# Optimization experiments

Measured on AMD Instinct MI355X. Metric: run time of the kernel, lower is better.

Reference implementation:

```python
import jax, jax.numpy as jnp
import numpy as np

B, C, H, W = 4, 64, 64, 64


def setup_inputs() -> dict:
    key = jax.random.key(0)
    ks = jax.random.split(key, 9)
    s = 1.0 / np.sqrt(C)
    return {
        "x1": jax.random.normal(ks[0], (B, C, H, W), dtype=jnp.float32),
        "x2": jax.random.normal(ks[1], (B, C, H, W), dtype=jnp.float32),
        "wq": jax.random.normal(ks[2], (C, C), dtype=jnp.float32) * s,
        "bq": jax.random.normal(ks[3], (C,), dtype=jnp.float32) * 0.01,
        "wk": jax.random.normal(ks[4], (C, C), dtype=jnp.float32) * s,
        "bk": jax.random.normal(ks[5], (C,), dtype=jnp.float32) * 0.01,
        "wv": jax.random.normal(ks[6], (C, C), dtype=jnp.float32) * s,
        "bv": jax.random.normal(ks[7], (C,), dtype=jnp.float32) * 0.01,
        "gamma": jax.random.normal(ks[8], (1,), dtype=jnp.float32) * 0.1,
    }


def _conv1x1(x, w, b):
    # 1x1 conv == per-pixel GEMM: [B,C,H,W] x [Cout,Cin] -> [B,Cout,H,W]
    return jnp.einsum('bchw,oc->bohw', x, w) + b[None, :, None, None]


def reference(x1, x2, wq, bq, wk, bk, wv, bv, gamma):
    b, c, h, w = x1.shape
    n = h * w
    q = _conv1x1(x1, wq, bq).reshape(b, c, n)   # [B,C,N]
    k = _conv1x1(x2, wk, bk).reshape(b, c, n)   # [B,C,N]
    v = _conv1x1(x2, wv, bv).reshape(b, c, n)   # [B,C,N]
    # attention[b,i,j] = sum_c q[b,c,i] * k[b,c,j]  -> [B,N,N]
    attn = jnp.einsum('bci,bcj->bij', q, k)
    attn = jax.nn.softmax(attn, axis=-1)
    # out[b,c,i] = sum_j v[b,c,j] * attn[b,i,j]
    out = jnp.einsum('bcj,bij->bci', v, attn).reshape(b, c, h, w)
    return gamma[0] * out + x1
```

## Files before the change

### kernel.cpp

```cpp
#include <hip/hip_runtime.h>
#include <cstdint>
#include <cstddef>


typedef __bf16 bf16x4 __attribute__((ext_vector_type(4)));
typedef __bf16 bf16x8 __attribute__((ext_vector_type(8)));
typedef float  f32x4  __attribute__((ext_vector_type(4)));
typedef float  f32x16 __attribute__((ext_vector_type(16)));
typedef short  s16x4  __attribute__((ext_vector_type(4)));

constexpr int C = 64;
constexpr int N = 4096;
constexpr float LOG2E = 1.44269504088896340736f;
constexpr float EXPSHIFT = 48.0f * 1.44269504088896340736f;

static __device__ __forceinline__ f32x4 mfma16(bf16x8 a, bf16x8 b, f32x4 c) {
    return __builtin_amdgcn_mfma_f32_16x16x32_bf16(a, b, c, 0, 0, 0);
}
static __device__ __forceinline__ f32x16 mfma32(bf16x8 a, bf16x8 b, f32x16 c) {
    return __builtin_amdgcn_mfma_f32_32x32x16_bf16(a, b, c, 0, 0, 0);
}
static __device__ __forceinline__ f32x16 pv_mfma(bf16x4 a, bf16x4 b, f32x16 c) {
#if __has_builtin(__builtin_amdgcn_mfma_f32_32x32x8bf16_1k)
    union U { bf16x4 h; s16x4 s; };
    U ua; ua.h = a;
    U ub; ub.h = b;
    return __builtin_amdgcn_mfma_f32_32x32x8bf16_1k(ua.s, ub.s, c, 0, 0, 0);
#else
    const __bf16 z = (__bf16)0.0f;
    bf16x8 a8 = {a[0], a[1], a[2], a[3], z, z, z, z};
    bf16x8 b8 = {b[0], b[1], b[2], b[3], z, z, z, z};
    return __builtin_amdgcn_mfma_f32_32x32x16_bf16(a8, b8, c, 0, 0, 0);
#endif
}
static __device__ __forceinline__ float fast_exp2(float x) {
#if __has_builtin(__builtin_amdgcn_exp2f)
    return __builtin_amdgcn_exp2f(x);
#else
    return exp2f(x);
#endif
}

__global__ __launch_bounds__(256) void qkv_kernel(
    const float* __restrict__ x1, const float* __restrict__ x2,
    const float* __restrict__ wq, const float* __restrict__ bq,
    const float* __restrict__ wk, const float* __restrict__ bk,
    const float* __restrict__ wv, const float* __restrict__ bv,
    __bf16* __restrict__ qo, __bf16* __restrict__ ko, __bf16* __restrict__ vo)
{
    __shared__ __bf16 wl[3][64][72];

    const int tid   = threadIdx.x;
    const int b     = blockIdx.x >> 6;
    const int nbase = (blockIdx.x & 63) * 64;

    {
        const float* wp[3] = {wq, wk, wv};
#pragma unroll
        for (int m = 0; m < 3; ++m)
#pragma unroll
            for (int i = 0; i < 4; ++i) {
                int idx = i * 256 + tid;
                int row = idx >> 4, c4 = (idx & 15) * 4;
                float4 a = *(const float4*)(wp[m] + row * 64 + c4);
                bf16x4 h = {(__bf16)a.x, (__bf16)a.y, (__bf16)a.z, (__bf16)a.w};
                *(bf16x4*)&wl[m][row][c4] = h;
            }
    }
    __syncthreads();

    const int wave = tid >> 6, lane = tid & 63;
    const int l = lane & 15, qd = lane >> 4;
    const int p = nbase + wave * 16 + l;

    const float* x1b = x1 + (size_t)b * C * N + p;
    const float* x2b = x2 + (size_t)b * C * N + p;
    bf16x8 ax1[2], ax2[2];
#pragma unroll
    for (int ks = 0; ks < 2; ++ks)
#pragma unroll
        for (int j = 0; j < 8; ++j) {
            int c = ks * 32 + qd * 8 + j;
            ax1[ks][j] = (__bf16)x1b[(size_t)c * N];
            ax2[ks][j] = (__bf16)x2b[(size_t)c * N];
        }

    const size_t tb = ((size_t)b * 128 + (nbase >> 5) + (wave >> 1)) * 2048;

#pragma unroll
    for (int ot = 0; ot < 4; ++ot) {
        const float bqv = bq[ot * 16 + l];
        const float bkv = bk[ot * 16 + l];
        f32x4 aq = {bqv, bqv, bqv, bqv};
        f32x4 ak = {bkv, bkv, bkv, bkv};
#pragma unroll
        for (int ks = 0; ks < 2; ++ks) {
            bf16x8 bwq = *(const bf16x8*)&wl[0][ot * 16 + l][ks * 32 + qd * 8];
            bf16x8 bwk = *(const bf16x8*)&wl[1][ot * 16 + l][ks * 32 + qd * 8];
            aq = mfma16(ax1[ks], bwq, aq);
            ak = mfma16(ax2[ks], bwk, ak);
        }
#pragma unroll
        for (int r = 0; r < 4; ++r) {
            int p32 = (wave & 1) * 16 + qd * 4 + r;
            size_t idx = tb + ot * 512 + (l >> 3) * 256 + p32 * 8 + (l & 7);
            qo[idx] = (__bf16)(aq[r] * LOG2E);
            ko[idx] = (__bf16)ak[r];
        }
    }

    const int kcs = ((wave & 1) * 16 + l) >> 3;
    const int vhi = (l >> 2) & 1;
#pragma unroll
    for (int ct = 0; ct < 4; ++ct) {
        f32x4 av;
#pragma unroll
        for (int r = 0; r < 4; ++r) av[r] = bv[ct * 16 + qd * 4 + r];
#pragma unroll
        for (int ks = 0; ks < 2; ++ks) {
            bf16x8 awv = *(const bf16x8*)&wl[2][ct * 16 + l][ks * 32 + qd * 8];
            av = mfma16(awv, ax2[ks], av);
        }
#pragma unroll
        for (int r = 0; r < 4; ++r) {
            int o = ct * 16 + qd * 4 + r;
            vo[tb + kcs * 512 + vhi * 256 + o * 4 + (l & 3)] = (__bf16)av[r];
        }
    }
}

__global__ __launch_bounds__(512, 2) void attn_kernel(
    const __bf16* __restrict__ qg, const __bf16* __restrict__ kg,
    const __bf16* __restrict__ vg, const float* __restrict__ x1,
    const float* __restrict__ gamma, float* __restrict__ out)
{
    __shared__ float lds_acc[3][64][64];
    __shared__ float lds_l[8][64];

    const int bid = blockIdx.x;
    const int xcd = bid & 7;
    const int b   = xcd >> 1;
    const int rt  = ((bid >> 3) << 1) | (xcd & 1);
    const int ibase = rt * 64;

    const int tid  = threadIdx.x;
    const int wave = tid >> 6, lane = tid & 63;
    const int il = lane & 31, hi = lane >> 5;

    const __bf16* qt = qg + ((size_t)b * 128 + rt * 2) * 2048;
    const __bf16* kt = kg + (size_t)b * 128 * 2048 + (size_t)(wave * 16) * 2048;
    const __bf16* vt = vg + (size_t)b * 128 * 2048 + (size_t)(wave * 16) * 2048;

    bf16x8 bqf[2][4];
#pragma unroll
    for (int qs = 0; qs < 2; ++qs)
#pragma unroll
        for (int kc = 0; kc < 4; ++kc)
            bqf[qs][kc] = *(const bf16x8*)(qt + qs * 2048 + kc * 512 + lane * 8);

    f32x16 accO[4];
#pragma unroll
    for (int a = 0; a < 4; ++a)
#pragma unroll
        for (int r = 0; r < 16; ++r) accO[a][r] = 0.f;
    float lsum[2] = {0.f, 0.f};

    bf16x8 akf[2][4];
    bf16x4 avf[2][4];

#pragma unroll
    for (int kc = 0; kc < 4; ++kc)
        akf[0][kc] = *(const bf16x8*)(kt + kc * 512 + lane * 8);

#pragma unroll 4
    for (int t = 0; t < 16; ++t) {
        const int cur = t & 1;
        if (t < 15) {
#pragma unroll
            for (int kc = 0; kc < 4; ++kc)
                akf[cur ^ 1][kc] = *(const bf16x8*)(kt + (size_t)(t + 1) * 2048 + kc * 512 + lane * 8);
        }
#pragma unroll
        for (int ct = 0; ct < 2; ++ct)
#pragma unroll
            for (int kcs = 0; kcs < 4; ++kcs)
                avf[ct][kcs] = *(const bf16x4*)(vt + (size_t)t * 2048 + kcs * 512 + hi * 256 + ct * 128 + il * 4);

#pragma unroll
        for (int qs = 0; qs < 2; ++qs) {
            f32x16 st;
#pragma unroll
            for (int r = 0; r < 16; ++r) st[r] = 0.f;
#pragma unroll
            for (int kc = 0; kc < 4; ++kc) st = mfma32(akf[cur][kc], bqf[qs][kc], st);

            bf16x4 bp[4];
            float ls = 0.f;
#pragma unroll
            for (int r = 0; r < 16; ++r) {
                float pv = fast_exp2(st[r] - EXPSHIFT);
                ls += pv;
                bp[r >> 2][r & 3] = (__bf16)pv;
            }
            lsum[qs] += ls;

#pragma unroll
            for (int ct = 0; ct < 2; ++ct)
#pragma unroll
                for (int kcs = 0; kcs < 4; ++kcs)
                    accO[qs * 2 + ct] = pv_mfma(avf[ct][kcs], bp[kcs], accO[qs * 2 + ct]);
        }
    }

#pragma unroll
    for (int qs = 0; qs < 2; ++qs) lsum[qs] += __shfl_xor(lsum[qs], 32);
    if (hi == 0) {
        lds_l[wave][il]      = lsum[0];
        lds_l[wave][32 + il] = lsum[1];
    }

#define ACC_STORE(SLOT)                                                        \
    do {                                                                       \
        _Pragma("unroll")                                                      \
        for (int qs = 0; qs < 2; ++qs)                                         \
            _Pragma("unroll")                                                  \
            for (int ct = 0; ct < 2; ++ct)                                     \
                _Pragma("unroll")                                              \
                for (int r = 0; r < 16; ++r)                                   \
                    lds_acc[SLOT][ct * 32 + (r & 3) + 8 * (r >> 2) + 4 * hi][qs * 32 + il] = accO[qs * 2 + ct][r]; \
    } while (0)
#define ACC_LOAD(SLOT)                                                         \
    do {                                                                       \
        _Pragma("unroll")                                                      \
        for (int qs = 0; qs < 2; ++qs)                                         \
            _Pragma("unroll")                                                  \
            for (int ct = 0; ct < 2; ++ct)                                     \
                _Pragma("unroll")                                              \
                for (int r = 0; r < 16; ++r)                                   \
                    accO[qs * 2 + ct][r] += lds_acc[SLOT][ct * 32 + (r & 3) + 8 * (r >> 2) + 4 * hi][qs * 32 + il]; \
    } while (0)

    if (wave >= 5) ACC_STORE(wave - 5);
    __syncthreads();
    if (wave >= 1 && wave <= 3) ACC_LOAD(wave - 1);
    __syncthreads();
    if (wave >= 2 && wave <= 4) ACC_STORE(wave - 2);
    __syncthreads();
    if (wave <= 1) ACC_LOAD(wave);
    if (wave == 0) ACC_LOAD(2);
    __syncthreads();
    if (wave == 1) ACC_STORE(0);
    __syncthreads();
    if (wave == 0) { ACC_LOAD(0); ACC_STORE(0); }
    __syncthreads();
#undef ACC_STORE
#undef ACC_LOAD

    const float g = gamma[0];
    {
        const int c  = tid >> 3;
        const int i8 = (tid & 7) * 8;
        float lv[8];
#pragma unroll
        for (int e = 0; e < 8; ++e) {
            float s = 0.f;
#pragma unroll
            for (int w = 0; w < 8; ++w) s += lds_l[w][i8 + e];
            lv[e] = s;
        }
        const size_t idx = ((size_t)b * C + c) * N + ibase + i8;
        f32x4 o0 = *(const f32x4*)&lds_acc[0][c][i8];
        f32x4 o1 = *(const f32x4*)&lds_acc[0][c][i8 + 4];
        f32x4 x0 = *(const f32x4*)(x1 + idx);
        f32x4 x4 = *(const f32x4*)(x1 + idx + 4);
        f32x4 r0, r1;
#pragma unroll
        for (int e = 0; e < 4; ++e) {
            r0[e] = g * o0[e] / lv[e] + x0[e];
            r1[e] = g * o1[e] / lv[4 + e] + x4[e];
        }
        *(f32x4*)(out + idx) = r0;
        *(f32x4*)(out + idx + 4) = r1;
    }
}

extern "C" void kernel_launch(void* const* d_in, const int* in_sizes, int n_in,
                              void* d_out, int out_size, void* d_ws, size_t ws_size,
                              hipStream_t stream) {
    const float* x1    = (const float*)d_in[0];
    const float* x2    = (const float*)d_in[1];
    const float* wq    = (const float*)d_in[2];
    const float* bqv   = (const float*)d_in[3];
    const float* wk    = (const float*)d_in[4];
    const float* bkv   = (const float*)d_in[5];
    const float* wv    = (const float*)d_in[6];
    const float* bvv   = (const float*)d_in[7];
    const float* gamma = (const float*)d_in[8];
    float* out = (float*)d_out;

    __bf16* qws = (__bf16*)d_ws;
    __bf16* kws = qws + (size_t)4 * 128 * 2048;
    __bf16* vws = kws + (size_t)4 * 128 * 2048;

    qkv_kernel<<<256, 256, 0, stream>>>(x1, x2, wq, bqv, wk, bkv, wv, bvv, qws, kws, vws);
    attn_kernel<<<256, 512, 0, stream>>>(qws, kws, vws, x1, gamma, out);
}
```

Measured before the change: 104.6 us.

## Split attention KV range across blocks and reduce partials in an epilogue kernel

The attention kernel moves from 256 blocks of 8 waves, each covering all keys for one 64-query tile, to 1024 blocks of 4 waves, each covering a quarter of the keys. Each block writes unnormalized partial outputs and row sums to workspace, and a new epilogue kernel sums the four splits, normalizes, and applies the gamma residual. Q fragments are now staged through LDS rather than held in registers, which lowers register pressure so three blocks can fit per CU. The goal is more parallelism and occupancy. The cost is an extra kernel launch, about 16MB of partial-output traffic through global memory, and extra LDS reads for Q.

```diff
diff --git a/kernel.cpp b/kernel.cpp
--- a/kernel.cpp
+++ b/kernel.cpp
@@ -129,34 +129,36 @@
     }
 }
 
-__global__ __launch_bounds__(512, 2) void attn_kernel(
+__global__ __launch_bounds__(256, 3) void attn_kernel(
     const __bf16* __restrict__ qg, const __bf16* __restrict__ kg,
-    const __bf16* __restrict__ vg, const float* __restrict__ x1,
-    const float* __restrict__ gamma, float* __restrict__ out)
+    const __bf16* __restrict__ vg,
+    float* __restrict__ partO, float* __restrict__ partL)
 {
-    __shared__ float lds_acc[3][64][64];
-    __shared__ float lds_l[8][64];
-
-    const int bid = blockIdx.x;
-    const int xcd = bid & 7;
-    const int b   = xcd >> 1;
-    const int rt  = ((bid >> 3) << 1) | (xcd & 1);
-    const int ibase = rt * 64;
+    __shared__ __bf16 lds_q[4096];
+    __shared__ float  lds_s[2][64][64];
+    __shared__ float  lds_l[4][64];
+
+    const int bid   = blockIdx.x;
+    const int xcd   = bid & 7;
+    const int b     = xcd >> 1;
+    const int local = ((bid >> 3) << 1) | (xcd & 1);
+    const int lqt   = local >> 2;
+    const int split = local & 3;
+    const int qt    = b * 64 + lqt;
 
     const int tid  = threadIdx.x;
     const int wave = tid >> 6, lane = tid & 63;
     const int il = lane & 31, hi = lane >> 5;
 
-    const __bf16* qt = qg + ((size_t)b * 128 + rt * 2) * 2048;
-    const __bf16* kt = kg + (size_t)b * 128 * 2048 + (size_t)(wave * 16) * 2048;
-    const __bf16* vt = vg + (size_t)b * 128 * 2048 + (size_t)(wave * 16) * 2048;
-
-    bf16x8 bqf[2][4];
-#pragma unroll
-    for (int qs = 0; qs < 2; ++qs)
-#pragma unroll
-        for (int kc = 0; kc < 4; ++kc)
-            bqf[qs][kc] = *(const bf16x8*)(qt + qs * 2048 + kc * 512 + lane * 8);
+    {
+        const __bf16* qsrc = qg + ((size_t)b * 128 + lqt * 2) * 2048;
+        *(bf16x8*)&lds_q[tid * 16]     = *(const bf16x8*)(qsrc + tid * 16);
+        *(bf16x8*)&lds_q[tid * 16 + 8] = *(const bf16x8*)(qsrc + tid * 16 + 8);
+    }
+    __syncthreads();
+
+    const __bf16* kt = kg + ((size_t)b * 128 + split * 32 + wave * 8) * 2048;
+    const __bf16* vt = vg + ((size_t)b * 128 + split * 32 + wave * 8) * 2048;
 
     f32x16 accO[4];
 #pragma unroll
@@ -172,10 +174,10 @@
     for (int kc = 0; kc < 4; ++kc)
         akf[0][kc] = *(const bf16x8*)(kt + kc * 512 + lane * 8);
 
-#pragma unroll 4
-    for (int t = 0; t < 16; ++t) {
+#pragma unroll 2
+    for (int t = 0; t < 8; ++t) {
         const int cur = t & 1;
-        if (t < 15) {
+        if (t < 7) {
 #pragma unroll
             for (int kc = 0; kc < 4; ++kc)
                 akf[cur ^ 1][kc] = *(const bf16x8*)(kt + (size_t)(t + 1) * 2048 + kc * 512 + lane * 8);
@@ -192,7 +194,10 @@
 #pragma unroll
             for (int r = 0; r < 16; ++r) st[r] = 0.f;
 #pragma unroll
-            for (int kc = 0; kc < 4; ++kc) st = mfma32(akf[cur][kc], bqf[qs][kc], st);
+            for (int kc = 0; kc < 4; ++kc) {
+                bf16x8 bqf = *(const bf16x8*)&lds_q[qs * 2048 + kc * 512 + lane * 8];
+                st = mfma32(akf[cur][kc], bqf, st);
+            }
 
             bf16x4 bp[4];
             float ls = 0.f;
@@ -212,8 +217,8 @@
         }
     }
 
-#pragma unroll
-    for (int qs = 0; qs < 2; ++qs) lsum[qs] += __shfl_xor(lsum[qs], 32);
+    lsum[0] += __shfl_xor(lsum[0], 32);
+    lsum[1] += __shfl_xor(lsum[1], 32);
     if (hi == 0) {
         lds_l[wave][il]      = lsum[0];
         lds_l[wave][32 + il] = lsum[1];
@@ -227,7 +232,7 @@
             for (int ct = 0; ct < 2; ++ct)                                     \
                 _Pragma("unroll")                                              \
                 for (int r = 0; r < 16; ++r)                                   \
-                    lds_acc[SLOT][ct * 32 + (r & 3) + 8 * (r >> 2) + 4 * hi][qs * 32 + il] = accO[qs * 2 + ct][r]; \
+                    lds_s[SLOT][ct * 32 + (r & 3) + 8 * (r >> 2) + 4 * hi][qs * 32 + il] = accO[qs * 2 + ct][r]; \
     } while (0)
 #define ACC_LOAD(SLOT)                                                         \
     do {                                                                       \
@@ -237,50 +242,74 @@
             for (int ct = 0; ct < 2; ++ct)                                     \
                 _Pragma("unroll")                                              \
                 for (int r = 0; r < 16; ++r)                                   \
-                    accO[qs * 2 + ct][r] += lds_acc[SLOT][ct * 32 + (r & 3) + 8 * (r >> 2) + 4 * hi][qs * 32 + il]; \
+                    accO[qs * 2 + ct][r] += lds_s[SLOT][ct * 32 + (r & 3) + 8 * (r >> 2) + 4 * hi][qs * 32 + il]; \
     } while (0)
 
-    if (wave >= 5) ACC_STORE(wave - 5);
-    __syncthreads();
-    if (wave >= 1 && wave <= 3) ACC_LOAD(wave - 1);
-    __syncthreads();
-    if (wave >= 2 && wave <= 4) ACC_STORE(wave - 2);
-    __syncthreads();
-    if (wave <= 1) ACC_LOAD(wave);
-    if (wave == 0) ACC_LOAD(2);
+    if (wave == 2) ACC_STORE(0);
+    if (wave == 3) ACC_STORE(1);
+    __syncthreads();
+    if (wave == 0) ACC_LOAD(0);
+    if (wave == 1) ACC_LOAD(1);
     __syncthreads();
     if (wave == 1) ACC_STORE(0);
     __syncthreads();
-    if (wave == 0) { ACC_LOAD(0); ACC_STORE(0); }
-    __syncthreads();
+    if (wave == 0) {
+        ACC_LOAD(0);
+        float* po = partO + (size_t)(qt * 4 + split) * 64 * 64;
+#pragma unroll
+        for (int qs = 0; qs < 2; ++qs)
+#pragma unroll
+            for (int ct = 0; ct < 2; ++ct)
+#pragma unroll
+                for (int r = 0; r < 16; ++r)
+                    po[(ct * 32 + (r & 3) + 8 * (r >> 2) + 4 * hi) * 64 + qs * 32 + il] = accO[qs * 2 + ct][r];
+        if (hi == 0) {
+            float s0 = lds_l[0][il] + lds_l[1][il] + lds_l[2][il] + lds_l[3][il];
+            float s1 = lds_l[0][32 + il] + lds_l[1][32 + il] + lds_l[2][32 + il] + lds_l[3][32 + il];
+            partL[(qt * 4 + split) * 64 + il]      = s0;
+            partL[(qt * 4 + split) * 64 + 32 + il] = s1;
+        }
+    }
 #undef ACC_STORE
 #undef ACC_LOAD
-
+}
+
+__global__ __launch_bounds__(256) void epilogue_kernel(
+    const float* __restrict__ partO, const float* __restrict__ partL,
+    const float* __restrict__ x1, const float* __restrict__ gamma,
+    float* __restrict__ out)
+{
+    __shared__ float lsum[64];
+    const int qt  = blockIdx.x;
+    const int tid = threadIdx.x;
+
+    if (tid < 64) {
+        float s = 0.f;
+#pragma unroll
+        for (int sp = 0; sp < 4; ++sp) s += partL[(qt * 4 + sp) * 64 + tid];
+        lsum[tid] = s;
+    }
+    __syncthreads();
+
+    const int c  = tid >> 2;
+    const int ig = (tid & 3) * 16;
+    const int b  = qt >> 6;
+    const int ibase = (qt & 63) * 64;
     const float g = gamma[0];
-    {
-        const int c  = tid >> 3;
-        const int i8 = (tid & 7) * 8;
-        float lv[8];
-#pragma unroll
-        for (int e = 0; e < 8; ++e) {
-            float s = 0.f;
-#pragma unroll
-            for (int w = 0; w < 8; ++w) s += lds_l[w][i8 + e];
-            lv[e] = s;
-        }
-        const size_t idx = ((size_t)b * C + c) * N + ibase + i8;
-        f32x4 o0 = *(const f32x4*)&lds_acc[0][c][i8];
-        f32x4 o1 = *(const f32x4*)&lds_acc[0][c][i8 + 4];
-        f32x4 x0 = *(const f32x4*)(x1 + idx);
-        f32x4 x4 = *(const f32x4*)(x1 + idx + 4);
-        f32x4 r0, r1;
-#pragma unroll
-        for (int e = 0; e < 4; ++e) {
-            r0[e] = g * o0[e] / lv[e] + x0[e];
-            r1[e] = g * o1[e] / lv[4 + e] + x4[e];
-        }
-        *(f32x4*)(out + idx) = r0;
-        *(f32x4*)(out + idx + 4) = r1;
+    const size_t obase = ((size_t)b * C + c) * N + ibase + ig;
+
+#pragma unroll
+    for (int e4 = 0; e4 < 4; ++e4) {
+        f32x4 acc = {0.f, 0.f, 0.f, 0.f};
+#pragma unroll
+        for (int sp = 0; sp < 4; ++sp)
+            acc += *(const f32x4*)&partO[((size_t)(qt * 4 + sp) * 64 + c) * 64 + ig + e4 * 4];
+        f32x4 xv = *(const f32x4*)(x1 + obase + e4 * 4);
+        f32x4 res;
+#pragma unroll
+        for (int e = 0; e < 4; ++e)
+            res[e] = g * acc[e] / lsum[ig + e4 * 4 + e] + xv[e];
+        *(f32x4*)(out + obase + e4 * 4) = res;
     }
 }
 
@@ -301,7 +330,10 @@
     __bf16* qws = (__bf16*)d_ws;
     __bf16* kws = qws + (size_t)4 * 128 * 2048;
     __bf16* vws = kws + (size_t)4 * 128 * 2048;
+    float*  partO = (float*)(vws + (size_t)4 * 128 * 2048);
+    float*  partL = partO + (size_t)256 * 4 * 64 * 64;
 
     qkv_kernel<<<256, 256, 0, stream>>>(x1, x2, wq, bqv, wk, bkv, wv, bvv, qws, kws, vws);
-    attn_kernel<<<256, 512, 0, stream>>>(qws, kws, vws, x1, gamma, out);
-}
+    attn_kernel<<<1024, 256, 0, stream>>>(qws, kws, vws, partO, partL);
+    epilogue_kernel<<<256, 256, 0, stream>>>(partO, partL, x1, gamma, out);
+}
```

Result: slower. 136.8 us (+30.8%).
